# Kernel optimization log

Hardware: AMD Instinct MI355X
Metric: run time of the kernel (lower is better)

## Reference

```python
import jax, jax.numpy as jnp
import numpy as np

# TT factorization for fc1: 768 = 4*4*6*8 -> 3072 = 4*6*8*16, ranks (1,12,24,12,1)
# TT factorization for fc2: 3072 = 4*6*8*16 -> 768 = 4*4*6*8, ranks (1,12,24,12,1)
IN_F1, OUT_F1 = (4, 4, 6, 8), (4, 6, 8, 16)
IN_F2, OUT_F2 = (4, 6, 8, 16), (4, 4, 6, 8)
RANKS = (12, 24, 12)


def _core(key, shape, fan_in):
    return jax.random.normal(key, shape, dtype=jnp.float32) * (fan_in ** -0.5)


def make_tt_params(key, in_f, out_f, ranks):
    r = (1,) + tuple(ranks) + (1,)
    ks = jax.random.split(key, 5)
    # boundary cores squeeze the unit rank dims
    g1 = _core(ks[0], (in_f[0], out_f[0], r[1]), in_f[0])              # (i1,o1,r1)
    g2 = _core(ks[1], (r[1], in_f[1], out_f[1], r[2]), r[1] * in_f[1])  # (r1,i2,o2,r2)
    g3 = _core(ks[2], (r[2], in_f[2], out_f[2], r[3]), r[2] * in_f[2])  # (r2,i3,o3,r3)
    g4 = _core(ks[3], (r[3], in_f[3], out_f[3]), r[3] * in_f[3])        # (r3,i4,o4)
    b = jnp.zeros((int(np.prod(out_f)),), dtype=jnp.float32)
    return g1, g2, g3, g4, b


def tt_linear(x2d, g1, g2, g3, g4, bias, in_f):
    # x2d: (N, prod(in_f)) -> (N, prod(out_f))
    z = x2d.reshape((-1,) + tuple(in_f))                  # (b,i1,i2,i3,i4)
    z = jnp.einsum('bijkl,ipr->bjklpr', z, g1)            # (b,i2,i3,i4,o1,r1)
    z = jnp.einsum('bjklpr,rjqs->bklpqs', z, g2)          # (b,i3,i4,o1,o2,r2)
    z = jnp.einsum('bklpqs,sktu->blpqtu', z, g3)          # (b,i4,o1,o2,o3,r3)
    z = jnp.einsum('blpqtu,ulv->bpqtv', z, g4)            # (b,o1,o2,o3,o4)
    return z.reshape(z.shape[0], -1) + bias


def setup_inputs() -> dict:
    key = jax.random.key(0)
    kx, k1, k2 = jax.random.split(key, 3)
    x = jax.random.normal(kx, (2, 2048, 768), dtype=jnp.float32)
    g1a, g1b, g1c, g1d, b1 = make_tt_params(k1, IN_F1, OUT_F1, RANKS)
    g2a, g2b, g2c, g2d, b2 = make_tt_params(k2, IN_F2, OUT_F2, RANKS)
    return {"x": x, "g1a": g1a, "g1b": g1b, "g1c": g1c, "g1d": g1d, "b1": b1,
            "g2a": g2a, "g2b": g2b, "g2c": g2c, "g2d": g2d, "b2": b2}


def reference(x, g1a, g1b, g1c, g1d, b1, g2a, g2b, g2c, g2d, b2):
    B, S, D = x.shape
    h = tt_linear(x.reshape(-1, D), g1a, g1b, g1c, g1d, b1, IN_F1)  # (N, 3072)
    h = jax.nn.gelu(h, approximate=False)  # nn.GELU() default = exact erf
    # dropout: identity in eval mode
    y = tt_linear(h, g2a, g2b, g2c, g2d, b2, IN_F2)                 # (N, 768)
    return y.reshape(B, S, -1)
```

## Files before the change

kernel.cpp:

```cpp
#include <hip/hip_runtime.h>
#include <cstdint>
#include <cstddef>

typedef unsigned short u16;
typedef __attribute__((ext_vector_type(8))) __bf16 bf16x8;
typedef __attribute__((ext_vector_type(4))) float f32x4;

__device__ __forceinline__ u16 f2bf(float f) {
  unsigned u = __float_as_uint(f);
  u += 0x7FFFu + ((u >> 16) & 1u);
  return (u16)(u >> 16);
}

__device__ __forceinline__ float bf2f(u16 h) {
  return __uint_as_float(((unsigned)h) << 16);
}

__device__ __forceinline__ void async16(u16* lds, const u16* g) {
  __builtin_amdgcn_global_load_lds(
      (const __attribute__((address_space(1))) unsigned int*)g,
      (__attribute__((address_space(3))) unsigned int*)lds, 16, 0, 0);
}

__global__ __launch_bounds__(256)
void prep(const float4* __restrict__ x4, ushort4* __restrict__ xb4,
          const float* __restrict__ gA1, const float* __restrict__ gB1,
          const float* __restrict__ gC1, const float* __restrict__ gD1,
          const float* __restrict__ gA2, const float* __restrict__ gB2,
          const float* __restrict__ gC2, const float* __restrict__ gD2,
          float* __restrict__ B12_1, float* __restrict__ B12_2,
          float* __restrict__ C1, float* __restrict__ C2) {
  const int b = blockIdx.x;
  const int tid = threadIdx.x;
  if (b < 3072) {
    int i = b * 256 + tid;
    float4 v = x4[i];
    ushort4 o;
    o.x = f2bf(v.x); o.y = f2bf(v.y); o.z = f2bf(v.z); o.w = f2bf(v.w);
    xb4[i] = o;
    return;
  }
  int idx = (b - 3072) * 256 + tid;
  if (idx < 9216) {
    int e = idx;
    int r2 = e % 24; int t = e / 24;
    int fo12 = t % 24, fi12 = t / 24;
    int i2 = fi12 % 4, i1 = fi12 / 4;
    int o2 = fo12 % 6, o1 = fo12 / 6;
    float s = 0.f;
#pragma unroll
    for (int r1 = 0; r1 < 12; ++r1)
      s += gA1[(i1 * 4 + o1) * 12 + r1] * gB1[((r1 * 4 + i2) * 6 + o2) * 24 + r2];
    B12_1[e] = s;
  } else if (idx < 18432) {
    int e = idx - 9216;
    int r2 = e % 24; int t = e / 24;
    int fo12 = t % 16, fi12 = t / 16;
    int i2 = fi12 % 6, i1 = fi12 / 6;
    int o2 = fo12 % 4, o1 = fo12 / 4;
    float s = 0.f;
#pragma unroll
    for (int r1 = 0; r1 < 12; ++r1)
      s += gA2[(i1 * 4 + o1) * 12 + r1] * gB2[((r1 * 6 + i2) * 4 + o2) * 24 + r2];
    B12_2[e] = s;
  } else if (idx < 165888) {
    int e = idx - 18432;
    int fi34 = e % 48; int t = e / 48;
    int fo34 = t % 128;
    int i3 = fi34 / 8, i4 = fi34 % 8;
    int o3 = fo34 / 16, o4 = fo34 % 16;
    int r2 = t / 128;
    float s = 0.f;
#pragma unroll
    for (int r3 = 0; r3 < 12; ++r3)
      s += gC1[((r2 * 6 + i3) * 8 + o3) * 12 + r3] * gD1[(r3 * 8 + i4) * 16 + o4];
    C1[e] = s;
  } else {
    int e = idx - 165888;
    int fi34 = e % 128; int t = e / 128;
    int fo34 = t % 48;
    int i3 = fi34 / 16, i4 = fi34 % 16;
    int o3 = fo34 / 8, o4 = fo34 % 8;
    int r2 = t / 48;
    float s = 0.f;
#pragma unroll
    for (int r3 = 0; r3 < 12; ++r3)
      s += gC2[((r2 * 8 + i3) * 6 + o3) * 12 + r3] * gD2[(r3 * 16 + i4) * 8 + o4];
    C2[e] = s;
  }
}

template <int FI12, int I34, int O12, int O34, int OG>
__device__ __forceinline__
void tt_expand_body(const float* __restrict__ B12, const float* __restrict__ C34t,
                    u16* __restrict__ Wt, int bx, int by, int tid, float* sB) {
  constexpr int R2 = 24;
  constexpr int Kin = FI12 * I34;
  constexpr int IC = Kin / 8;
  constexpr int I34C = I34 / 8;
  for (int e = tid; e < FI12 * OG * R2; e += 256) {
    int r2 = e % R2; int t = e / R2;
    int f = t % OG; int fi12 = t / OG;
    sB[(fi12 * OG + f) * 25 + r2] = B12[(fi12 * O12 + by * OG + f) * R2 + r2];
  }
  __syncthreads();
  const int t = bx * 256 + tid;
  const int fo34 = t / IC;
  const int ic = t % IC;
  const int fi12 = ic / I34C;
  const int fi34 = (ic % I34C) * 8;

  float acc[OG][8];
#pragma unroll
  for (int f = 0; f < OG; ++f)
#pragma unroll
    for (int k = 0; k < 8; ++k) acc[f][k] = 0.f;

  for (int r2 = 0; r2 < R2; ++r2) {
    const float4* cp = (const float4*)(C34t + ((size_t)(r2 * O34 + fo34) * I34 + fi34));
    float4 c0 = cp[0], c1 = cp[1];
    float c[8] = {c0.x, c0.y, c0.z, c0.w, c1.x, c1.y, c1.z, c1.w};
#pragma unroll
    for (int f = 0; f < OG; ++f) {
      float bb = sB[(fi12 * OG + f) * 25 + r2];
#pragma unroll
      for (int k = 0; k < 8; ++k) acc[f][k] += bb * c[k];
    }
  }
#pragma unroll
  for (int f = 0; f < OG; ++f) {
    int out = (by * OG + f) * O34 + fo34;
    u16 v[8];
#pragma unroll
    for (int k = 0; k < 8; ++k) v[k] = f2bf(acc[f][k]);
    *(uint4*)(Wt + (size_t)out * Kin + fi12 * I34 + fi34) = *(const uint4*)v;
  }
}

__global__ __launch_bounds__(256)
void tt_expand2(const float* __restrict__ B12_1, const float* __restrict__ C1, u16* __restrict__ W1t,
                const float* __restrict__ B12_2, const float* __restrict__ C2, u16* __restrict__ W2t) {
  __shared__ float sB[24 * 4 * 25];
  const int b = blockIdx.x;
  const int tid = threadIdx.x;
  if (b < 288) {
    tt_expand_body<16, 48, 24, 128, 4>(B12_1, C1, W1t, b % 48, b / 48, tid, sB);
  } else {
    int bb = b - 288;
    tt_expand_body<24, 128, 16, 48, 4>(B12_2, C2, W2t, bb % 72, bb / 72, tid, sB);
  }
}

template <int EPI, int MAP, int NT>
__global__ __launch_bounds__(256, 2)
void gemm_bt(const u16* __restrict__ A, const u16* __restrict__ Bt,
             const float* __restrict__ bias, u16* __restrict__ Out,
             float* __restrict__ OutF, int N, int lda, int ldb) {
  const int flat = blockIdx.x;
  const int xcd = flat & 7;
  const int local = flat >> 3;
  int bm, bn, bz;
  if (MAP == 1) {
    bm = (xcd >> 1) * 8 + (local & 7);
    bn = (xcd & 1) * 16 + (local >> 3);
    bz = 0;
  } else {
    bz = xcd & 1;
    bm = (xcd >> 1) * 8 + (local & 7);
    bn = local >> 3;
  }
  const int kbeg = (MAP == 2) ? bz * 1536 : 0;

  __shared__ __align__(16) u16 AL[2][8192];
  __shared__ __align__(16) u16 BL[3][6144];

  const int tid = threadIdx.x;
  const int wave = tid >> 6, lane = tid & 63;
  const int lr = lane & 15, lq = lane >> 4;
  const int wm = (wave & 1) * 64;
  const int wn = (wave >> 1) * 48;

  const int prow = tid >> 3;
  const int pcc  = (tid & 7) ^ (prow & 7);
  const u16* Ag = A + (size_t)(bm * 128 + prow) * lda + kbeg + pcc * 8;
  const u16* Bg = Bt + (size_t)(bn * 96 + prow) * ldb + kbeg + pcc * 8;

  auto stA = [&](int slot, int p, int k) {
    async16(&AL[slot][0] + p * 2048 + tid * 8, Ag + (size_t)(p * 32) * lda + k);
  };
  auto stB = [&](int slot, int p, int k) {
    async16(&BL[slot][0] + p * 2048 + tid * 8, Bg + (size_t)(p * 32) * ldb + k);
  };

  int aOff[2][4], bOff[2][3];
#pragma unroll
  for (int kk = 0; kk < 2; ++kk) {
#pragma unroll
    for (int mi = 0; mi < 4; ++mi) {
      int L = (wm + mi * 16 + lr) * 128 + kk * 64 + lq * 16;
      L ^= ((L >> 7) & 7) << 4;
      aOff[kk][mi] = L >> 1;
    }
#pragma unroll
    for (int nj = 0; nj < 3; ++nj) {
      int L = (wn + nj * 16 + lr) * 128 + kk * 64 + lq * 16;
      L ^= ((L >> 7) & 7) << 4;
      bOff[kk][nj] = L >> 1;
    }
  }

  f32x4 acc[4][3];
#pragma unroll
  for (int mi = 0; mi < 4; ++mi)
#pragma unroll
    for (int nj = 0; nj < 3; ++nj) acc[mi][nj] = (f32x4){0.f, 0.f, 0.f, 0.f};

  stA(0, 0, 0); stA(0, 1, 0); stA(0, 2, 0); stA(0, 3, 0);
  stB(0, 0, 0); stB(0, 1, 0); stB(0, 2, 0);
  stB(1, 0, 64); stB(1, 1, 64); stB(1, 2, 64);
  asm volatile("s_waitcnt vmcnt(3)" ::: "memory");
  __builtin_amdgcn_s_barrier();
  __builtin_amdgcn_sched_barrier(0);

  int bsR = 0, bsW = 2;
  for (int t = 0; t < NT; ++t) {
    const u16* Ab = &AL[t & 1][0];
    const u16* Bb = &BL[bsR][0];
    const int wAs = (t + 1) & 1;
    const int kA = ((t + 1 < NT) ? t + 1 : NT - 1) * 64;
    const int kB = ((t + 2 < NT) ? t + 2 : NT - 1) * 64;

    bf16x8 bf[3], af[4];
#pragma unroll
    for (int nj = 0; nj < 3; ++nj) bf[nj] = *(const bf16x8*)(Bb + bOff[0][nj]);
#pragma unroll
    for (int mi = 0; mi < 4; ++mi) af[mi] = *(const bf16x8*)(Ab + aOff[0][mi]);
    stA(wAs, 0, kA); stA(wAs, 1, kA); stA(wAs, 2, kA); stA(wAs, 3, kA);
    __builtin_amdgcn_s_barrier();
    asm volatile("s_waitcnt lgkmcnt(0)" ::: "memory");
    __builtin_amdgcn_sched_barrier(0);
    __builtin_amdgcn_s_setprio(1);
#pragma unroll
    for (int mi = 0; mi < 4; ++mi)
#pragma unroll
      for (int nj = 0; nj < 3; ++nj)
        acc[mi][nj] = __builtin_amdgcn_mfma_f32_16x16x32_bf16(af[mi], bf[nj], acc[mi][nj], 0, 0, 0);
    __builtin_amdgcn_s_setprio(0);
    __builtin_amdgcn_s_barrier();
    __builtin_amdgcn_sched_barrier(0);
#pragma unroll
    for (int nj = 0; nj < 3; ++nj) bf[nj] = *(const bf16x8*)(Bb + bOff[1][nj]);
#pragma unroll
    for (int mi = 0; mi < 4; ++mi) af[mi] = *(const bf16x8*)(Ab + aOff[1][mi]);
    stB(bsW, 0, kB); stB(bsW, 1, kB); stB(bsW, 2, kB);
    __builtin_amdgcn_s_barrier();
    asm volatile("s_waitcnt lgkmcnt(0)" ::: "memory");
    __builtin_amdgcn_sched_barrier(0);
    __builtin_amdgcn_s_setprio(1);
#pragma unroll
    for (int mi = 0; mi < 4; ++mi)
#pragma unroll
      for (int nj = 0; nj < 3; ++nj)
        acc[mi][nj] = __builtin_amdgcn_mfma_f32_16x16x32_bf16(af[mi], bf[nj], acc[mi][nj], 0, 0, 0);
    __builtin_amdgcn_s_setprio(0);
    asm volatile("s_waitcnt vmcnt(3)" ::: "memory");
    __builtin_amdgcn_s_barrier();
    __builtin_amdgcn_sched_barrier(0);

    bsR = (bsR + 1 == 3) ? 0 : bsR + 1;
    bsW = (bsW + 1 == 3) ? 0 : bsW + 1;
  }

  const int r0 = bm * 128 + wm + lq * 4;
  const int c0 = bn * 96 + wn + lr;
  if (EPI == 0) {
    float bv[3];
#pragma unroll
    for (int nj = 0; nj < 3; ++nj) bv[nj] = bias[c0 + nj * 16];
#pragma unroll
    for (int mi = 0; mi < 4; ++mi) {
#pragma unroll
      for (int r = 0; r < 4; ++r) {
        const size_t rowoff = (size_t)(r0 + mi * 16 + r) * N;
#pragma unroll
        for (int nj = 0; nj < 3; ++nj) {
          float v = acc[mi][nj][r] + bv[nj];
          float inner = v * fmaf(v * v, 0.0356774081f, 0.7978845608f);
          float e = __builtin_amdgcn_exp2f(2.8853900818f * inner);
          float r1 = __builtin_amdgcn_rcpf(1.0f + e);
          v = v - v * r1;
          Out[rowoff + c0 + nj * 16] = f2bf(v);
        }
      }
    }
  } else {
    float bv[3];
#pragma unroll
    for (int nj = 0; nj < 3; ++nj) bv[nj] = (bz == 0) ? bias[c0 + nj * 16] : 0.f;
#pragma unroll
    for (int mi = 0; mi < 4; ++mi) {
#pragma unroll
      for (int r = 0; r < 4; ++r) {
        const size_t rowoff = (size_t)(r0 + mi * 16 + r) * N;
#pragma unroll
        for (int nj = 0; nj < 3; ++nj)
          atomicAdd(OutF + rowoff + c0 + nj * 16, acc[mi][nj][r] + bv[nj]);
      }
    }
  }
}

extern "C" void kernel_launch(void* const* d_in, const int* in_sizes, int n_in,
                              void* d_out, int out_size, void* d_ws, size_t ws_size,
                              hipStream_t stream) {
  const float* x   = (const float*)d_in[0];
  const float* g1a = (const float*)d_in[1];
  const float* g1b = (const float*)d_in[2];
  const float* g1c = (const float*)d_in[3];
  const float* g1d = (const float*)d_in[4];
  const float* b1  = (const float*)d_in[5];
  const float* g2a = (const float*)d_in[6];
  const float* g2b = (const float*)d_in[7];
  const float* g2c = (const float*)d_in[8];
  const float* g2d = (const float*)d_in[9];
  const float* b2  = (const float*)d_in[10];
  float* out = (float*)d_out;

  char* ws = (char*)d_ws;
  u16* xb   = (u16*)(ws + 0);
  u16* W1t  = (u16*)(ws + 6291456);
  u16* W2t  = (u16*)(ws + 11010048);
  u16* h    = (u16*)(ws + 15728640);
  float* B12_1 = (float*)(ws + 40894464);
  float* B12_2 = (float*)(ws + 40894464 + 36864);
  float* C1    = (float*)(ws + 40894464 + 73728);
  float* C2    = (float*)(ws + 40894464 + 663552);

  prep<<<4296, 256, 0, stream>>>((const float4*)x, (ushort4*)xb,
                                 g1a, g1b, g1c, g1d, g2a, g2b, g2c, g2d,
                                 B12_1, B12_2, C1, C2);

  tt_expand2<<<576, 256, 0, stream>>>(B12_1, C1, W1t, B12_2, C2, W2t);

  gemm_bt<0, 1, 12><<<1024, 256, 0, stream>>>(xb, W1t, b1, h, nullptr, 3072, 768, 768);
  gemm_bt<1, 2, 24><<<512, 256, 0, stream>>>(h, W2t, b2, nullptr, out, 768, 3072, 3072);
}
```

Measured before the change: 171.3 us.

## Drop split-K atomics in second GEMM and stage epilogue through LDS

The second GEMM no longer splits K across two blocks that merge with float atomicAdd. Each of 256 blocks now runs the full K range (48 tiles) and writes its output directly. Both GEMMs now stage results through a shared LDS buffer, which lets them write coalesced vector stores of packed bf16 or float4 instead of scattered scalar stores. In exchange, the second GEMM launches half as many blocks with twice the serial K loop. The 98-float row stride also makes the 16-byte LDS reads only 8-byte aligned on odd rows.

```diff
diff --git a/kernel.cpp b/kernel.cpp
--- a/kernel.cpp
+++ b/kernel.cpp
@@ -159,20 +159,16 @@
   const int flat = blockIdx.x;
   const int xcd = flat & 7;
   const int local = flat >> 3;
-  int bm, bn, bz;
+  int bm, bn;
   if (MAP == 1) {
     bm = (xcd >> 1) * 8 + (local & 7);
     bn = (xcd & 1) * 16 + (local >> 3);
-    bz = 0;
   } else {
-    bz = xcd & 1;
     bm = (xcd >> 1) * 8 + (local & 7);
-    bn = local >> 3;
-  }
-  const int kbeg = (MAP == 2) ? bz * 1536 : 0;
-
-  __shared__ __align__(16) u16 AL[2][8192];
-  __shared__ __align__(16) u16 BL[3][6144];
+    bn = (xcd & 1) * 4 + (local >> 3);
+  }
+
+  __shared__ __align__(16) u16 SH[34816];
 
   const int tid = threadIdx.x;
   const int wave = tid >> 6, lane = tid & 63;
@@ -182,14 +178,14 @@
 
   const int prow = tid >> 3;
   const int pcc  = (tid & 7) ^ (prow & 7);
-  const u16* Ag = A + (size_t)(bm * 128 + prow) * lda + kbeg + pcc * 8;
-  const u16* Bg = Bt + (size_t)(bn * 96 + prow) * ldb + kbeg + pcc * 8;
+  const u16* Ag = A + (size_t)(bm * 128 + prow) * lda + pcc * 8;
+  const u16* Bg = Bt + (size_t)(bn * 96 + prow) * ldb + pcc * 8;
 
   auto stA = [&](int slot, int p, int k) {
-    async16(&AL[slot][0] + p * 2048 + tid * 8, Ag + (size_t)(p * 32) * lda + k);
+    async16(&SH[0] + slot * 8192 + p * 2048 + tid * 8, Ag + (size_t)(p * 32) * lda + k);
   };
   auto stB = [&](int slot, int p, int k) {
-    async16(&BL[slot][0] + p * 2048 + tid * 8, Bg + (size_t)(p * 32) * ldb + k);
+    async16(&SH[16384] + slot * 6144 + p * 2048 + tid * 8, Bg + (size_t)(p * 32) * ldb + k);
   };
 
   int aOff[2][4], bOff[2][3];
@@ -224,8 +220,8 @@
 
   int bsR = 0, bsW = 2;
   for (int t = 0; t < NT; ++t) {
-    const u16* Ab = &AL[t & 1][0];
-    const u16* Bb = &BL[bsR][0];
+    const u16* Ab = &SH[0] + (t & 1) * 8192;
+    const u16* Bb = &SH[16384] + bsR * 6144;
     const int wAs = (t + 1) & 1;
     const int kA = ((t + 1 < NT) ? t + 1 : NT - 1) * 64;
     const int kB = ((t + 2 < NT) ? t + 2 : NT - 1) * 64;
@@ -271,41 +267,45 @@
     bsW = (bsW + 1 == 3) ? 0 : bsW + 1;
   }
 
-  const int r0 = bm * 128 + wm + lq * 4;
-  const int c0 = bn * 96 + wn + lr;
-  if (EPI == 0) {
-    float bv[3];
-#pragma unroll
-    for (int nj = 0; nj < 3; ++nj) bv[nj] = bias[c0 + nj * 16];
-#pragma unroll
-    for (int mi = 0; mi < 4; ++mi) {
-#pragma unroll
-      for (int r = 0; r < 4; ++r) {
-        const size_t rowoff = (size_t)(r0 + mi * 16 + r) * N;
-#pragma unroll
-        for (int nj = 0; nj < 3; ++nj) {
-          float v = acc[mi][nj][r] + bv[nj];
+  asm volatile("s_waitcnt vmcnt(0)" ::: "memory");
+  __syncthreads();
+
+  float* CS = (float*)&SH[0];
+  const int r0l = wm + lq * 4;
+  const int c0l = wn + lr;
+  float bv[3];
+#pragma unroll
+  for (int nj = 0; nj < 3; ++nj) bv[nj] = bias[bn * 96 + c0l + nj * 16];
+#pragma unroll
+  for (int mi = 0; mi < 4; ++mi) {
+#pragma unroll
+    for (int r = 0; r < 4; ++r) {
+#pragma unroll
+      for (int nj = 0; nj < 3; ++nj) {
+        float v = acc[mi][nj][r] + bv[nj];
+        if (EPI == 0) {
           float inner = v * fmaf(v * v, 0.0356774081f, 0.7978845608f);
           float e = __builtin_amdgcn_exp2f(2.8853900818f * inner);
           float r1 = __builtin_amdgcn_rcpf(1.0f + e);
           v = v - v * r1;
-          Out[rowoff + c0 + nj * 16] = f2bf(v);
         }
+        CS[(r0l + mi * 16 + r) * 98 + c0l + nj * 16] = v;
       }
     }
-  } else {
-    float bv[3];
-#pragma unroll
-    for (int nj = 0; nj < 3; ++nj) bv[nj] = (bz == 0) ? bias[c0 + nj * 16] : 0.f;
-#pragma unroll
-    for (int mi = 0; mi < 4; ++mi) {
-#pragma unroll
-      for (int r = 0; r < 4; ++r) {
-        const size_t rowoff = (size_t)(r0 + mi * 16 + r) * N;
-#pragma unroll
-        for (int nj = 0; nj < 3; ++nj)
-          atomicAdd(OutF + rowoff + c0 + nj * 16, acc[mi][nj][r] + bv[nj]);
-      }
+  }
+  __syncthreads();
+#pragma unroll
+  for (int c = 0; c < 12; ++c) {
+    int chunk = c * 256 + tid;
+    int row = chunk / 24, col4 = chunk % 24;
+    f32x4 v = *(const f32x4*)&CS[row * 98 + col4 * 4];
+    if (EPI == 0) {
+      unsigned lo = (unsigned)f2bf(v[0]) | ((unsigned)f2bf(v[1]) << 16);
+      unsigned hi = (unsigned)f2bf(v[2]) | ((unsigned)f2bf(v[3]) << 16);
+      uint2 pk; pk.x = lo; pk.y = hi;
+      *(uint2*)(Out + (size_t)(bm * 128 + row) * N + bn * 96 + col4 * 4) = pk;
+    } else {
+      *(f32x4*)(OutF + (size_t)(bm * 128 + row) * N + bn * 96 + col4 * 4) = v;
     }
   }
 }
@@ -343,5 +343,5 @@
   tt_expand2<<<576, 256, 0, stream>>>(B12_1, C1, W1t, B12_2, C2, W2t);
 
   gemm_bt<0, 1, 12><<<1024, 256, 0, stream>>>(xb, W1t, b1, h, nullptr, 3072, 768, 768);
-  gemm_bt<1, 2, 24><<<512, 256, 0, stream>>>(h, W2t, b2, nullptr, out, 768, 3072, 3072);
-}
+  gemm_bt<1, 2, 48><<<256, 256, 0, stream>>>(h, W2t, b2, nullptr, out, 768, 3072, 3072);
+}
```

Result: no change. 170.0 us (-0.7%).

## Replace split-K atomics in fc2 GEMM with BM=64 tiles and drop mid-loop barriers

Applied to the files above, without the earlier changes.

The second GEMM no longer splits K across two blocks with float atomicAdd. It uses 64-row M tiles over the full K (NT=48), so the 512 blocks each write their output directly with plain stores. The main loop is restructured to load both k-halves into separate register sets and removes the intermediate s_barrier/waitcnt between the two MFMA phases, keeping only one sync per iteration. This removes the atomic traffic and the need for a zeroed output, but each block now runs a longer K loop with a smaller tile. The reduced synchronization may also risk LDS read/write hazards.

```diff
diff --git a/kernel.cpp b/kernel.cpp
--- a/kernel.cpp
+++ b/kernel.cpp
@@ -151,39 +151,39 @@
   }
 }
 
-template <int EPI, int MAP, int NT>
+template <int EPI, int MAP, int NT, int BM>
 __global__ __launch_bounds__(256, 2)
 void gemm_bt(const u16* __restrict__ A, const u16* __restrict__ Bt,
              const float* __restrict__ bias, u16* __restrict__ Out,
              float* __restrict__ OutF, int N, int lda, int ldb) {
+  constexpr int MI = BM / 32;
+  constexpr int PA = BM / 32;
+  constexpr int ASLOT = BM * 64;
   const int flat = blockIdx.x;
   const int xcd = flat & 7;
   const int local = flat >> 3;
-  int bm, bn, bz;
+  int bm, bn;
   if (MAP == 1) {
     bm = (xcd >> 1) * 8 + (local & 7);
     bn = (xcd & 1) * 16 + (local >> 3);
-    bz = 0;
   } else {
-    bz = xcd & 1;
-    bm = (xcd >> 1) * 8 + (local & 7);
+    bm = xcd * 8 + (local & 7);
     bn = local >> 3;
   }
-  const int kbeg = (MAP == 2) ? bz * 1536 : 0;
-
-  __shared__ __align__(16) u16 AL[2][8192];
+
+  __shared__ __align__(16) u16 AL[2][ASLOT];
   __shared__ __align__(16) u16 BL[3][6144];
 
   const int tid = threadIdx.x;
   const int wave = tid >> 6, lane = tid & 63;
   const int lr = lane & 15, lq = lane >> 4;
-  const int wm = (wave & 1) * 64;
+  const int wm = (wave & 1) * (BM / 2);
   const int wn = (wave >> 1) * 48;
 
   const int prow = tid >> 3;
   const int pcc  = (tid & 7) ^ (prow & 7);
-  const u16* Ag = A + (size_t)(bm * 128 + prow) * lda + kbeg + pcc * 8;
-  const u16* Bg = Bt + (size_t)(bn * 96 + prow) * ldb + kbeg + pcc * 8;
+  const u16* Ag = A + (size_t)(bm * BM + prow) * lda + pcc * 8;
+  const u16* Bg = Bt + (size_t)(bn * 96 + prow) * ldb + pcc * 8;
 
   auto stA = [&](int slot, int p, int k) {
     async16(&AL[slot][0] + p * 2048 + tid * 8, Ag + (size_t)(p * 32) * lda + k);
@@ -192,11 +192,11 @@
     async16(&BL[slot][0] + p * 2048 + tid * 8, Bg + (size_t)(p * 32) * ldb + k);
   };
 
-  int aOff[2][4], bOff[2][3];
+  int aOff[2][MI], bOff[2][3];
 #pragma unroll
   for (int kk = 0; kk < 2; ++kk) {
 #pragma unroll
-    for (int mi = 0; mi < 4; ++mi) {
+    for (int mi = 0; mi < MI; ++mi) {
       int L = (wm + mi * 16 + lr) * 128 + kk * 64 + lq * 16;
       L ^= ((L >> 7) & 7) << 4;
       aOff[kk][mi] = L >> 1;
@@ -209,13 +209,14 @@
     }
   }
 
-  f32x4 acc[4][3];
-#pragma unroll
-  for (int mi = 0; mi < 4; ++mi)
+  f32x4 acc[MI][3];
+#pragma unroll
+  for (int mi = 0; mi < MI; ++mi)
 #pragma unroll
     for (int nj = 0; nj < 3; ++nj) acc[mi][nj] = (f32x4){0.f, 0.f, 0.f, 0.f};
 
-  stA(0, 0, 0); stA(0, 1, 0); stA(0, 2, 0); stA(0, 3, 0);
+#pragma unroll
+  for (int p = 0; p < PA; ++p) stA(0, p, 0);
   stB(0, 0, 0); stB(0, 1, 0); stB(0, 2, 0);
   stB(1, 0, 64); stB(1, 1, 64); stB(1, 2, 64);
   asm volatile("s_waitcnt vmcnt(3)" ::: "memory");
@@ -230,39 +231,34 @@
     const int kA = ((t + 1 < NT) ? t + 1 : NT - 1) * 64;
     const int kB = ((t + 2 < NT) ? t + 2 : NT - 1) * 64;
 
-    bf16x8 bf[3], af[4];
-#pragma unroll
-    for (int nj = 0; nj < 3; ++nj) bf[nj] = *(const bf16x8*)(Bb + bOff[0][nj]);
-#pragma unroll
-    for (int mi = 0; mi < 4; ++mi) af[mi] = *(const bf16x8*)(Ab + aOff[0][mi]);
-    stA(wAs, 0, kA); stA(wAs, 1, kA); stA(wAs, 2, kA); stA(wAs, 3, kA);
-    __builtin_amdgcn_s_barrier();
+    bf16x8 a0[MI], b0[3], a1[MI], b1[3];
+#pragma unroll
+    for (int nj = 0; nj < 3; ++nj) b0[nj] = *(const bf16x8*)(Bb + bOff[0][nj]);
+#pragma unroll
+    for (int mi = 0; mi < MI; ++mi) a0[mi] = *(const bf16x8*)(Ab + aOff[0][mi]);
+#pragma unroll
+    for (int p = 0; p < PA; ++p) stA(wAs, p, kA);
+    __builtin_amdgcn_s_setprio(1);
+#pragma unroll
+    for (int mi = 0; mi < MI; ++mi)
+#pragma unroll
+      for (int nj = 0; nj < 3; ++nj)
+        acc[mi][nj] = __builtin_amdgcn_mfma_f32_16x16x32_bf16(a0[mi], b0[nj], acc[mi][nj], 0, 0, 0);
+    __builtin_amdgcn_s_setprio(0);
+#pragma unroll
+    for (int nj = 0; nj < 3; ++nj) b1[nj] = *(const bf16x8*)(Bb + bOff[1][nj]);
+#pragma unroll
+    for (int mi = 0; mi < MI; ++mi) a1[mi] = *(const bf16x8*)(Ab + aOff[1][mi]);
+    stB(bsW, 0, kB); stB(bsW, 1, kB); stB(bsW, 2, kB);
+    __builtin_amdgcn_s_setprio(1);
+#pragma unroll
+    for (int mi = 0; mi < MI; ++mi)
+#pragma unroll
+      for (int nj = 0; nj < 3; ++nj)
+        acc[mi][nj] = __builtin_amdgcn_mfma_f32_16x16x32_bf16(a1[mi], b1[nj], acc[mi][nj], 0, 0, 0);
+    __builtin_amdgcn_s_setprio(0);
     asm volatile("s_waitcnt lgkmcnt(0)" ::: "memory");
     __builtin_amdgcn_sched_barrier(0);
-    __builtin_amdgcn_s_setprio(1);
-#pragma unroll
-    for (int mi = 0; mi < 4; ++mi)
-#pragma unroll
-      for (int nj = 0; nj < 3; ++nj)
-        acc[mi][nj] = __builtin_amdgcn_mfma_f32_16x16x32_bf16(af[mi], bf[nj], acc[mi][nj], 0, 0, 0);
-    __builtin_amdgcn_s_setprio(0);
-    __builtin_amdgcn_s_barrier();
-    __builtin_amdgcn_sched_barrier(0);
-#pragma unroll
-    for (int nj = 0; nj < 3; ++nj) bf[nj] = *(const bf16x8*)(Bb + bOff[1][nj]);
-#pragma unroll
-    for (int mi = 0; mi < 4; ++mi) af[mi] = *(const bf16x8*)(Ab + aOff[1][mi]);
-    stB(bsW, 0, kB); stB(bsW, 1, kB); stB(bsW, 2, kB);
-    __builtin_amdgcn_s_barrier();
-    asm volatile("s_waitcnt lgkmcnt(0)" ::: "memory");
-    __builtin_amdgcn_sched_barrier(0);
-    __builtin_amdgcn_s_setprio(1);
-#pragma unroll
-    for (int mi = 0; mi < 4; ++mi)
-#pragma unroll
-      for (int nj = 0; nj < 3; ++nj)
-        acc[mi][nj] = __builtin_amdgcn_mfma_f32_16x16x32_bf16(af[mi], bf[nj], acc[mi][nj], 0, 0, 0);
-    __builtin_amdgcn_s_setprio(0);
     asm volatile("s_waitcnt vmcnt(3)" ::: "memory");
     __builtin_amdgcn_s_barrier();
     __builtin_amdgcn_sched_barrier(0);
@@ -271,40 +267,28 @@
     bsW = (bsW + 1 == 3) ? 0 : bsW + 1;
   }
 
-  const int r0 = bm * 128 + wm + lq * 4;
+  const int r0 = bm * BM + wm + lq * 4;
   const int c0 = bn * 96 + wn + lr;
-  if (EPI == 0) {
-    float bv[3];
-#pragma unroll
-    for (int nj = 0; nj < 3; ++nj) bv[nj] = bias[c0 + nj * 16];
-#pragma unroll
-    for (int mi = 0; mi < 4; ++mi) {
-#pragma unroll
-      for (int r = 0; r < 4; ++r) {
-        const size_t rowoff = (size_t)(r0 + mi * 16 + r) * N;
-#pragma unroll
-        for (int nj = 0; nj < 3; ++nj) {
-          float v = acc[mi][nj][r] + bv[nj];
+  float bv[3];
+#pragma unroll
+  for (int nj = 0; nj < 3; ++nj) bv[nj] = bias[c0 + nj * 16];
+#pragma unroll
+  for (int mi = 0; mi < MI; ++mi) {
+#pragma unroll
+    for (int r = 0; r < 4; ++r) {
+      const size_t rowoff = (size_t)(r0 + mi * 16 + r) * N;
+#pragma unroll
+      for (int nj = 0; nj < 3; ++nj) {
+        float v = acc[mi][nj][r] + bv[nj];
+        if (EPI == 0) {
           float inner = v * fmaf(v * v, 0.0356774081f, 0.7978845608f);
           float e = __builtin_amdgcn_exp2f(2.8853900818f * inner);
           float r1 = __builtin_amdgcn_rcpf(1.0f + e);
           v = v - v * r1;
           Out[rowoff + c0 + nj * 16] = f2bf(v);
+        } else {
+          OutF[rowoff + c0 + nj * 16] = v;
         }
-      }
-    }
-  } else {
-    float bv[3];
-#pragma unroll
-    for (int nj = 0; nj < 3; ++nj) bv[nj] = (bz == 0) ? bias[c0 + nj * 16] : 0.f;
-#pragma unroll
-    for (int mi = 0; mi < 4; ++mi) {
-#pragma unroll
-      for (int r = 0; r < 4; ++r) {
-        const size_t rowoff = (size_t)(r0 + mi * 16 + r) * N;
-#pragma unroll
-        for (int nj = 0; nj < 3; ++nj)
-          atomicAdd(OutF + rowoff + c0 + nj * 16, acc[mi][nj][r] + bv[nj]);
       }
     }
   }
@@ -342,6 +326,6 @@
 
   tt_expand2<<<576, 256, 0, stream>>>(B12_1, C1, W1t, B12_2, C2, W2t);
 
-  gemm_bt<0, 1, 12><<<1024, 256, 0, stream>>>(xb, W1t, b1, h, nullptr, 3072, 768, 768);
-  gemm_bt<1, 2, 24><<<512, 256, 0, stream>>>(h, W2t, b2, nullptr, out, 768, 3072, 3072);
-}
+  gemm_bt<0, 1, 12, 128><<<1024, 256, 0, stream>>>(xb, W1t, b1, h, nullptr, 3072, 768, 768);
+  gemm_bt<2, 3, 48, 64><<<512, 256, 0, stream>>>(h, W2t, b2, nullptr, out, 768, 3072, 3072);
+}
```

Result: faster. 162.9 us (-4.9%).
